# Kernel optimization log

Measured on AMD Instinct MI355X. Metric: run time of the kernel, lower is better.

Reference implementation:

```python
import jax, jax.numpy as jnp
import numpy as np

EMBED_DIM = 2048
NUM_HEADS = 16
HEAD_DIM = EMBED_DIM // NUM_HEADS
B, S = 1, 2048


def rotate_half(x):
    x1, x2 = jnp.split(x, 2, axis=-1)
    return jnp.concatenate((-x2, x1), axis=-1)


def setup_inputs() -> dict:
    key = jax.random.key(0)
    ks = jax.random.split(key, 8)
    scale = 1.0 / np.sqrt(EMBED_DIM)
    x = jax.random.normal(ks[0], (B, S, EMBED_DIM), dtype=jnp.float32)
    # realistic RoPE tables
    inv_freq = 1.0 / (10000.0 ** (jnp.arange(0, HEAD_DIM, 2, dtype=jnp.float32) / HEAD_DIM))
    t = jnp.arange(S, dtype=jnp.float32)
    freqs = jnp.outer(t, inv_freq)                      # [S, D/2]
    emb = jnp.concatenate((freqs, freqs), axis=-1)      # [S, D]
    rotary_cos = jnp.broadcast_to(jnp.cos(emb)[None], (B, S, HEAD_DIM))
    rotary_sin = jnp.broadcast_to(jnp.sin(emb)[None], (B, S, HEAD_DIM))
    Wq = jax.random.normal(ks[1], (EMBED_DIM, EMBED_DIM), dtype=jnp.float32) * scale
    Wk = jax.random.normal(ks[2], (EMBED_DIM, EMBED_DIM), dtype=jnp.float32) * scale
    Wv = jax.random.normal(ks[3], (EMBED_DIM, EMBED_DIM), dtype=jnp.float32) * scale
    Wo = jax.random.normal(ks[4], (EMBED_DIM, EMBED_DIM), dtype=jnp.float32) * scale
    return {"x": x, "rotary_cos": rotary_cos, "rotary_sin": rotary_sin,
            "Wq": Wq, "Wk": Wk, "Wv": Wv, "Wo": Wo}


def reference(x, rotary_cos, rotary_sin, Wq, Wk, Wv, Wo):
    b, s, e = x.shape
    h, d = NUM_HEADS, HEAD_DIM
    # QKV projections (nn.Linear: x @ W.T), reshape to [B, H, S, D]
    def proj(W):
        return jnp.einsum('bse,fe->bsf', x, W).reshape(b, s, h, d).transpose(0, 2, 1, 3)
    q, k, v = proj(Wq), proj(Wk), proj(Wv)
    # RoPE: cos/sin [B, S, D] -> [B, 1, S, D]
    cos = rotary_cos[:, None, :, :]
    sin = rotary_sin[:, None, :, :]
    q = q * cos + rotate_half(q) * sin
    k = k * cos + rotate_half(k) * sin
    # causal SDPA
    scores = jnp.einsum('bhqd,bhkd->bhqk', q, k) / jnp.sqrt(jnp.float32(d)).astype(x.dtype)
    causal = jnp.tril(jnp.ones((s, s), dtype=bool))
    scores = jnp.where(causal, scores, jnp.finfo(scores.dtype).min)
    attn = jax.nn.softmax(scores, axis=-1)
    out = jnp.einsum('bhqk,bhkd->bhqd', attn, v)
    out = out.transpose(0, 2, 1, 3).reshape(b, s, e)
    return jnp.einsum('bse,fe->bsf', out, Wo)
```

## Files before the change

### kernel.cpp

```cpp
#include <hip/hip_runtime.h>
#include <hip/hip_bf16.h>

#define S_LEN 2048
#define EMB   2048
#define NH    16
#define HD    128

typedef __attribute__((ext_vector_type(8))) __bf16 bf16x8;
typedef __attribute__((ext_vector_type(8))) unsigned short ushort8;
typedef __attribute__((ext_vector_type(4))) unsigned short ushort4v;
typedef __attribute__((ext_vector_type(4))) float  floatx4;

__device__ inline unsigned short f2b(float f) {
    __hip_bfloat16 h = __float2bfloat16(f);
    return *reinterpret_cast<unsigned short*>(&h);
}
__device__ inline float b2f(unsigned short u) {
    union { unsigned int i; float f; } c;
    c.i = ((unsigned int)u) << 16;
    return c.f;
}

__device__ inline ushort8 cvt16_lo(const float4& a, const float4& b) {
    ushort8 r;
    r[0] = f2b(a.x); r[1] = f2b(a.y); r[2] = f2b(a.z); r[3] = f2b(a.w);
    r[4] = f2b(b.x); r[5] = f2b(b.y); r[6] = f2b(b.z); r[7] = f2b(b.w);
    return r;
}

__global__ __launch_bounds__(256) void cvt_bf16x5(
    const float* __restrict__ s0, const float* __restrict__ s1,
    const float* __restrict__ s2, const float* __restrict__ s3,
    const float* __restrict__ s4,
    unsigned short* __restrict__ d0, unsigned short* __restrict__ d1,
    unsigned short* __restrict__ d2, unsigned short* __restrict__ d3,
    unsigned short* __restrict__ d4)
{
    const int i = blockIdx.x * 256 + threadIdx.x;
    const float* s; unsigned short* d;
    switch (blockIdx.y) {
        case 0: s = s0; d = d0; break;
        case 1: s = s1; d = d1; break;
        case 2: s = s2; d = d2; break;
        case 3: s = s3; d = d3; break;
        default: s = s4; d = d4; break;
    }
    float4 v = ((const float4*)s)[i];
    ushort4v r;
    r[0] = f2b(v.x); r[1] = f2b(v.y); r[2] = f2b(v.z); r[3] = f2b(v.w);
    ((ushort4v*)d)[i] = r;
}

template <int MODE, bool PRE>
__global__ __launch_bounds__(256) void gemm128(
    const void* __restrict__ Av,
    const void* __restrict__ B0v, const void* __restrict__ B1v,
    const void* __restrict__ B2v,
    float* __restrict__ outMN,
    __hip_bfloat16* __restrict__ qbuf, __hip_bfloat16* __restrict__ kbuf,
    __hip_bfloat16* __restrict__ vT,
    const float* __restrict__ rc, const float* __restrict__ rs)
{
    __shared__ union {
        struct { unsigned short A[128][40]; unsigned short B[128][40]; } s;
        unsigned short CtV[128][136];
        unsigned short CtR[128][137];
    } sm;

    const int m0 = blockIdx.x * 128;
    const int by = blockIdx.y;

    int widx = 0, hh = 0, n0 = 0;
    const void* Bv;
    if (MODE == 1) {
        widx = by >> 4;
        hh   = by & 15;
        n0   = hh * 128;
        Bv   = (widx == 0) ? B0v : (widx == 1) ? B1v : B2v;
    } else {
        n0 = by * 128;
        Bv = B0v;
    }

    const int t    = threadIdx.x;
    const int lane = t & 63;
    const int w    = t >> 6;
    const int l15  = lane & 15;
    const int g4   = lane >> 4;
    const int koff = g4 * 8;
    const int mw   = (w >> 1) * 64;
    const int nw   = (w & 1) * 64;

    const int srow = t >> 1;
    const int scol = (t & 1) * 16;

    const floatx4 z = {0.f, 0.f, 0.f, 0.f};
    floatx4 acc[4][4];
    #pragma unroll
    for (int i = 0; i < 4; i++)
        #pragma unroll
        for (int j = 0; j < 4; j++) acc[i][j] = z;

    const int K = EMB;
    for (int k0 = 0; k0 < K; k0 += 32) {
        ushort8 a0, a1, b0, b1;
        if (MODE == 0 || PRE) {
            const unsigned short* Ab = (const unsigned short*)Av;
            a0 = *(const ushort8*)(Ab + (size_t)(m0 + srow) * K + k0 + scol);
            a1 = *(const ushort8*)(Ab + (size_t)(m0 + srow) * K + k0 + scol + 8);
        } else {
            const float* Af = (const float*)Av;
            const float* ap = Af + (size_t)(m0 + srow) * K + k0 + scol;
            a0 = cvt16_lo(*(const float4*)(ap),     *(const float4*)(ap + 4));
            a1 = cvt16_lo(*(const float4*)(ap + 8), *(const float4*)(ap + 12));
        }
        if (PRE) {
            const unsigned short* Bb = (const unsigned short*)Bv;
            b0 = *(const ushort8*)(Bb + (size_t)(n0 + srow) * K + k0 + scol);
            b1 = *(const ushort8*)(Bb + (size_t)(n0 + srow) * K + k0 + scol + 8);
        } else {
            const float* Bf = (const float*)Bv;
            const float* bp = Bf + (size_t)(n0 + srow) * K + k0 + scol;
            b0 = cvt16_lo(*(const float4*)(bp),     *(const float4*)(bp + 4));
            b1 = cvt16_lo(*(const float4*)(bp + 8), *(const float4*)(bp + 12));
        }
        __syncthreads();
        *(ushort8*)&sm.s.A[srow][scol]     = a0;
        *(ushort8*)&sm.s.A[srow][scol + 8] = a1;
        *(ushort8*)&sm.s.B[srow][scol]     = b0;
        *(ushort8*)&sm.s.B[srow][scol + 8] = b1;
        __syncthreads();

        bf16x8 af[4], bg[4];
        #pragma unroll
        for (int i = 0; i < 4; i++)
            af[i] = *(const bf16x8*)&sm.s.A[mw + i * 16 + l15][koff];
        #pragma unroll
        for (int j = 0; j < 4; j++)
            bg[j] = *(const bf16x8*)&sm.s.B[nw + j * 16 + l15][koff];

        #pragma unroll
        for (int i = 0; i < 4; i++)
            #pragma unroll
            for (int j = 0; j < 4; j++)
                acc[i][j] = __builtin_amdgcn_mfma_f32_16x16x32_bf16(af[i], bg[j], acc[i][j], 0, 0, 0);
    }

    if (MODE == 0) {
        #pragma unroll
        for (int i = 0; i < 4; i++)
            #pragma unroll
            for (int j = 0; j < 4; j++)
                #pragma unroll
                for (int r = 0; r < 4; r++) {
                    int row = m0 + mw + i * 16 + g4 * 4 + r;
                    int col = n0 + nw + j * 16 + l15;
                    outMN[(size_t)row * EMB + col] = acc[i][j][r];
                }
    } else if (widx < 2) {
        __syncthreads();
        #pragma unroll
        for (int i = 0; i < 4; i++)
            #pragma unroll
            for (int j = 0; j < 4; j++)
                #pragma unroll
                for (int r = 0; r < 4; r++)
                    sm.CtR[nw + j * 16 + l15][mw + i * 16 + g4 * 4 + r] = f2b(acc[i][j][r]);
        __syncthreads();

        __hip_bfloat16* dst = (widx == 0) ? qbuf : kbuf;
        const int dd  = t & 127;
        const int sl0 = t >> 7;
        #pragma unroll 4
        for (int rep = 0; rep < 64; rep++) {
            const int sl = rep * 2 + sl0;
            const int s  = m0 + sl;
            const float c  = rc[(size_t)s * HD + dd];
            const float sn = rs[(size_t)s * HD + dd];
            const float x0 = b2f(sm.CtR[dd][sl]);
            const float xr = b2f(sm.CtR[dd ^ 64][sl]);
            const float rot = (dd < 64) ? -xr : xr;
            dst[((size_t)hh * S_LEN + s) * HD + dd] = __float2bfloat16(x0 * c + rot * sn);
        }
    } else {
        __syncthreads();
        #pragma unroll
        for (int i = 0; i < 4; i++)
            #pragma unroll
            for (int j = 0; j < 4; j++)
                #pragma unroll
                for (int r = 0; r < 4; r++)
                    sm.CtV[nw + j * 16 + l15][mw + i * 16 + g4 * 4 + r] = f2b(acc[i][j][r]);
        __syncthreads();
        const int dd = t >> 1;
        const int ms = (t & 1) * 64;
        __hip_bfloat16* dstv = vT + ((size_t)hh * HD + dd) * S_LEN + m0 + ms;
        #pragma unroll
        for (int c = 0; c < 8; c++)
            *(ushort8*)(dstv + c * 8) = *(const ushort8*)&sm.CtV[dd][ms + c * 8];
    }
}

__global__ __launch_bounds__(256) void flash_attn(
    const __hip_bfloat16* __restrict__ qb, const __hip_bfloat16* __restrict__ kb,
    const __hip_bfloat16* __restrict__ vT, __hip_bfloat16* __restrict__ attnb)
{
    __shared__ __align__(16) unsigned short Ks[64][136];
    __shared__ __align__(16) unsigned short Vs[128][72];
    __shared__ __align__(16) unsigned short Ps[4][16][72];

    const int bx = (gridDim.x - 1) - blockIdx.x;
    const int q0 = bx * 64;
    const int h  = blockIdx.y;
    const int t    = threadIdx.x;
    const int lane = t & 63;
    const int w    = t >> 6;
    const size_t hb  = (size_t)h * S_LEN;
    const size_t hbT = (size_t)h * HD;

    const int l15 = lane & 15;
    const int g4  = lane >> 4;
    const int koff = g4 * 8;

    const int kr = t >> 2;
    const int kc = (t & 3) * 32;
    const int vr = t >> 1;
    const int vc = (t & 1) * 32;

    bf16x8 qf[4];
    const __hip_bfloat16* qrow = qb + (hb + q0 + w * 16 + l15) * HD;
    #pragma unroll
    for (int kk = 0; kk < 4; kk++)
        qf[kk] = *(const bf16x8*)(qrow + kk * 32 + koff);

    const floatx4 z = {0.f, 0.f, 0.f, 0.f};
    floatx4 O[8] = {z, z, z, z, z, z, z, z};
    float lpart[4] = {0.f, 0.f, 0.f, 0.f};

    const float scale = 0.08838834764831845f;

    ushort8 krg[4], vrg[4];
    {
        const __hip_bfloat16* kg = kb + (hb + kr) * HD + kc;
        const __hip_bfloat16* vg = vT + (hbT + vr) * S_LEN + vc;
        #pragma unroll
        for (int c = 0; c < 4; c++) krg[c] = *(const ushort8*)(kg + c * 8);
        #pragma unroll
        for (int c = 0; c < 4; c++) vrg[c] = *(const ushort8*)(vg + c * 8);
    }

    for (int jb0 = 0; jb0 <= q0; jb0 += 64) {
        __syncthreads();
        #pragma unroll
        for (int c = 0; c < 4; c++) *(ushort8*)&Ks[kr][kc + c * 8] = krg[c];
        #pragma unroll
        for (int c = 0; c < 4; c++) *(ushort8*)&Vs[vr][vc + c * 8] = vrg[c];
        __syncthreads();

        if (jb0 + 64 <= q0) {
            const __hip_bfloat16* kg = kb + (hb + jb0 + 64 + kr) * HD + kc;
            const __hip_bfloat16* vg = vT + (hbT + vr) * S_LEN + jb0 + 64 + vc;
            #pragma unroll
            for (int c = 0; c < 4; c++) krg[c] = *(const ushort8*)(kg + c * 8);
            #pragma unroll
            for (int c = 0; c < 4; c++) vrg[c] = *(const ushort8*)(vg + c * 8);
        }

        floatx4 sc[4];
        #pragma unroll
        for (int jb = 0; jb < 4; jb++) {
            floatx4 acc = z;
            #pragma unroll
            for (int kk = 0; kk < 4; kk++) {
                bf16x8 kf = *(const bf16x8*)&Ks[jb * 16 + l15][kk * 32 + koff];
                acc = __builtin_amdgcn_mfma_f32_16x16x32_bf16(qf[kk], kf, acc, 0, 0, 0);
            }
            sc[jb] = acc;
        }

        const bool diag = (jb0 == q0);
        #pragma unroll
        for (int jb = 0; jb < 4; jb++)
            #pragma unroll
            for (int r = 0; r < 4; r++) {
                float s = sc[jb][r] * scale;
                if (diag && (jb * 16 + l15) > (w * 16 + g4 * 4 + r)) s = -1e30f;
                float p = __expf(s - 6.0f);
                sc[jb][r] = p;
                lpart[r] += p;
            }

        #pragma unroll
        for (int jb = 0; jb < 4; jb++)
            #pragma unroll
            for (int r = 0; r < 4; r++)
                Ps[w][g4 * 4 + r][jb * 16 + l15] = f2b(sc[jb][r]);

        #pragma unroll
        for (int half = 0; half < 2; half++) {
            bf16x8 af = *(const bf16x8*)&Ps[w][l15][half * 32 + koff];
            #pragma unroll
            for (int db = 0; db < 8; db++) {
                bf16x8 bf = *(const bf16x8*)&Vs[db * 16 + l15][half * 32 + koff];
                O[db] = __builtin_amdgcn_mfma_f32_16x16x32_bf16(af, bf, O[db], 0, 0, 0);
            }
        }
    }

    float inv[4];
    #pragma unroll
    for (int r = 0; r < 4; r++) {
        float s = lpart[r];
        #pragma unroll
        for (int o = 1; o < 16; o <<= 1) s += __shfl_xor(s, o, 64);
        inv[r] = 1.f / s;
    }

    #pragma unroll
    for (int db = 0; db < 8; db++)
        #pragma unroll
        for (int r = 0; r < 4; r++) {
            const int row = q0 + w * 16 + g4 * 4 + r;
            const int col = h * HD + db * 16 + l15;
            attnb[(size_t)row * EMB + col] = __float2bfloat16(O[db][r] * inv[r]);
        }
}

extern "C" void kernel_launch(void* const* d_in, const int* in_sizes, int n_in,
                              void* d_out, int out_size, void* d_ws, size_t ws_size,
                              hipStream_t stream) {
    const float* x  = (const float*)d_in[0];
    const float* rc = (const float*)d_in[1];
    const float* rs = (const float*)d_in[2];
    const float* Wq = (const float*)d_in[3];
    const float* Wk = (const float*)d_in[4];
    const float* Wv = (const float*)d_in[5];
    const float* Wo = (const float*)d_in[6];
    float* out = (float*)d_out;

    const size_t MB = 1u << 20;
    char* ws = (char*)d_ws;
    __hip_bfloat16* qbuf  = (__hip_bfloat16*)(ws);
    __hip_bfloat16* kbuf  = (__hip_bfloat16*)(ws +  8 * MB);
    __hip_bfloat16* vTbuf = (__hip_bfloat16*)(ws + 16 * MB);
    __hip_bfloat16* attnb = (__hip_bfloat16*)(ws + 24 * MB);

    const bool pre = (ws_size >= 72 * MB);

    if (pre) {
        unsigned short* xb  = (unsigned short*)(ws + 32 * MB);
        unsigned short* wqb = (unsigned short*)(ws + 40 * MB);
        unsigned short* wkb = (unsigned short*)(ws + 48 * MB);
        unsigned short* wvb = (unsigned short*)(ws + 56 * MB);
        unsigned short* wob = (unsigned short*)(ws + 64 * MB);

        hipLaunchKernelGGL(cvt_bf16x5, dim3(4096, 5), dim3(256), 0, stream,
                           x, Wq, Wk, Wv, Wo, xb, wqb, wkb, wvb, wob);

        hipLaunchKernelGGL((gemm128<1, true>), dim3(16, 48), dim3(256), 0, stream,
                           (const void*)xb, (const void*)wqb, (const void*)wkb,
                           (const void*)wvb, (float*)nullptr,
                           qbuf, kbuf, vTbuf, rc, rs);

        hipLaunchKernelGGL(flash_attn, dim3(S_LEN / 64, NH), dim3(256), 0, stream,
                           qbuf, kbuf, vTbuf, attnb);

        hipLaunchKernelGGL((gemm128<0, true>), dim3(16, 16), dim3(256), 0, stream,
                           (const void*)attnb, (const void*)wob, (const void*)nullptr,
                           (const void*)nullptr, out,
                           (__hip_bfloat16*)nullptr, (__hip_bfloat16*)nullptr,
                           (__hip_bfloat16*)nullptr, rc, rs);
    } else {
        hipLaunchKernelGGL((gemm128<1, false>), dim3(16, 48), dim3(256), 0, stream,
                           (const void*)x, (const void*)Wq, (const void*)Wk,
                           (const void*)Wv, (float*)nullptr,
                           qbuf, kbuf, vTbuf, rc, rs);

        hipLaunchKernelGGL(flash_attn, dim3(S_LEN / 64, NH), dim3(256), 0, stream,
                           qbuf, kbuf, vTbuf, attnb);

        hipLaunchKernelGGL((gemm128<0, false>), dim3(16, 16), dim3(256), 0, stream,
                           (const void*)attnb, (const void*)Wo, (const void*)nullptr,
                           (const void*)nullptr, out,
                           (__hip_bfloat16*)nullptr, (__hip_bfloat16*)nullptr,
                           (__hip_bfloat16*)nullptr, rc, rs);
    }
}
```

Before: 312.0 us.

## Use direct global-to-LDS loads with swizzle and split-K output projection

Replaces the register-staged tile loads in the pre-converted QKV and output GEMMs with global_load_lds direct-to-LDS transfers into an XOR-swizzled unpadded layout, cutting register traffic and LDS bank conflicts. The output projection is split along K into two halves that accumulate into a zeroed output with float atomics, doubling the block count to fill more CUs. This adds a memset and atomic-add traffic, makes the fp32 summation order nondeterministic, and still has no double buffering across the load/compute barrier.

```diff
diff --git a/kernel.cpp b/kernel.cpp
--- a/kernel.cpp
+++ b/kernel.cpp
@@ -26,6 +26,12 @@
     r[0] = f2b(a.x); r[1] = f2b(a.y); r[2] = f2b(a.z); r[3] = f2b(a.w);
     r[4] = f2b(b.x); r[5] = f2b(b.y); r[6] = f2b(b.z); r[7] = f2b(b.w);
     return r;
+}
+
+__device__ inline void gll16(const unsigned short* g, unsigned short* l) {
+    __builtin_amdgcn_global_load_lds(
+        (const __attribute__((address_space(1))) unsigned int*)g,
+        (__attribute__((address_space(3))) unsigned int*)l, 16, 0, 0);
 }
 
 __global__ __launch_bounds__(256) void cvt_bf16x5(
@@ -51,8 +57,190 @@
     ((ushort4v*)d)[i] = r;
 }
 
-template <int MODE, bool PRE>
-__global__ __launch_bounds__(256) void gemm128(
+
+__global__ __launch_bounds__(256) void gemm_qkv_async(
+    const unsigned short* __restrict__ Ab,
+    const unsigned short* __restrict__ Bq, const unsigned short* __restrict__ Bk,
+    const unsigned short* __restrict__ Bv,
+    __hip_bfloat16* __restrict__ qbuf, __hip_bfloat16* __restrict__ kbuf,
+    __hip_bfloat16* __restrict__ vT,
+    const float* __restrict__ rc, const float* __restrict__ rs)
+{
+    __shared__ __align__(16) union {
+        struct { unsigned short A[4096]; unsigned short B[4096]; } s;
+        unsigned short CtV[128][136];
+        unsigned short CtR[128][137];
+    } sm;
+
+    const int m0   = blockIdx.x * 128;
+    const int by   = blockIdx.y;
+    const int widx = by >> 4;
+    const int hh   = by & 15;
+    const int n0   = hh * 128;
+    const unsigned short* Bb = (widx == 0) ? Bq : (widx == 1) ? Bk : Bv;
+
+    const int t    = threadIdx.x;
+    const int lane = t & 63;
+    const int w    = t >> 6;
+    const int l15  = lane & 15;
+    const int g4   = lane >> 4;
+    const int mw   = (w >> 1) * 64;
+    const int nw   = (w & 1) * 64;
+
+    const int crow = lane >> 2;
+    const int clog = (lane & 3) ^ ((crow >> 1) & 3);
+    const int pc   = g4 ^ ((l15 >> 1) & 3);
+
+    const floatx4 z = {0.f, 0.f, 0.f, 0.f};
+    floatx4 acc[4][4];
+    #pragma unroll
+    for (int i = 0; i < 4; i++)
+        #pragma unroll
+        for (int j = 0; j < 4; j++) acc[i][j] = z;
+
+    const int K = EMB;
+    for (int k0 = 0; k0 < K; k0 += 32) {
+        __syncthreads();
+        #pragma unroll
+        for (int c = 0; c < 2; c++) {
+            const int ck  = w * 2 + c;
+            const int row = ck * 16 + crow;
+            gll16(Ab + (size_t)(m0 + row) * K + k0 + clog * 8, &sm.s.A[ck * 512]);
+            gll16(Bb + (size_t)(n0 + row) * K + k0 + clog * 8, &sm.s.B[ck * 512]);
+        }
+        __syncthreads();
+
+        bf16x8 af[4], bg[4];
+        #pragma unroll
+        for (int i = 0; i < 4; i++)
+            af[i] = *(const bf16x8*)&sm.s.A[(mw + i * 16 + l15) * 32 + pc * 8];
+        #pragma unroll
+        for (int j = 0; j < 4; j++)
+            bg[j] = *(const bf16x8*)&sm.s.B[(nw + j * 16 + l15) * 32 + pc * 8];
+
+        #pragma unroll
+        for (int i = 0; i < 4; i++)
+            #pragma unroll
+            for (int j = 0; j < 4; j++)
+                acc[i][j] = __builtin_amdgcn_mfma_f32_16x16x32_bf16(af[i], bg[j], acc[i][j], 0, 0, 0);
+    }
+
+    if (widx < 2) {
+        __syncthreads();
+        #pragma unroll
+        for (int i = 0; i < 4; i++)
+            #pragma unroll
+            for (int j = 0; j < 4; j++)
+                #pragma unroll
+                for (int r = 0; r < 4; r++)
+                    sm.CtR[nw + j * 16 + l15][mw + i * 16 + g4 * 4 + r] = f2b(acc[i][j][r]);
+        __syncthreads();
+
+        __hip_bfloat16* dst = (widx == 0) ? qbuf : kbuf;
+        const int dd  = t & 127;
+        const int sl0 = t >> 7;
+        #pragma unroll 4
+        for (int rep = 0; rep < 64; rep++) {
+            const int sl = rep * 2 + sl0;
+            const int s  = m0 + sl;
+            const float c  = rc[(size_t)s * HD + dd];
+            const float sn = rs[(size_t)s * HD + dd];
+            const float x0 = b2f(sm.CtR[dd][sl]);
+            const float xr = b2f(sm.CtR[dd ^ 64][sl]);
+            const float rot = (dd < 64) ? -xr : xr;
+            dst[((size_t)hh * S_LEN + s) * HD + dd] = __float2bfloat16(x0 * c + rot * sn);
+        }
+    } else {
+        __syncthreads();
+        #pragma unroll
+        for (int i = 0; i < 4; i++)
+            #pragma unroll
+            for (int j = 0; j < 4; j++)
+                #pragma unroll
+                for (int r = 0; r < 4; r++)
+                    sm.CtV[nw + j * 16 + l15][mw + i * 16 + g4 * 4 + r] = f2b(acc[i][j][r]);
+        __syncthreads();
+        const int dd = t >> 1;
+        const int ms = (t & 1) * 64;
+        __hip_bfloat16* dstv = vT + ((size_t)hh * HD + dd) * S_LEN + m0 + ms;
+        #pragma unroll
+        for (int c = 0; c < 8; c++)
+            *(ushort8*)(dstv + c * 8) = *(const ushort8*)&sm.CtV[dd][ms + c * 8];
+    }
+}
+
+__global__ __launch_bounds__(256) void gemm_wo_async(
+    const unsigned short* __restrict__ Ab,
+    const unsigned short* __restrict__ Bb,
+    float* __restrict__ outMN)
+{
+    __shared__ __align__(16) struct { unsigned short A[4096]; unsigned short B[4096]; } sm;
+
+    const int m0 = blockIdx.x * 128;
+    const int n0 = blockIdx.y * 128;
+    const int kz = blockIdx.z;
+
+    const int t    = threadIdx.x;
+    const int lane = t & 63;
+    const int w    = t >> 6;
+    const int l15  = lane & 15;
+    const int g4   = lane >> 4;
+    const int mw   = (w >> 1) * 64;
+    const int nw   = (w & 1) * 64;
+
+    const int crow = lane >> 2;
+    const int clog = (lane & 3) ^ ((crow >> 1) & 3);
+    const int pc   = g4 ^ ((l15 >> 1) & 3);
+
+    const floatx4 z = {0.f, 0.f, 0.f, 0.f};
+    floatx4 acc[4][4];
+    #pragma unroll
+    for (int i = 0; i < 4; i++)
+        #pragma unroll
+        for (int j = 0; j < 4; j++) acc[i][j] = z;
+
+    const int K = EMB;
+    const int kbeg = kz * (K / 2), kend = kbeg + K / 2;
+    for (int k0 = kbeg; k0 < kend; k0 += 32) {
+        __syncthreads();
+        #pragma unroll
+        for (int c = 0; c < 2; c++) {
+            const int ck  = w * 2 + c;
+            const int row = ck * 16 + crow;
+            gll16(Ab + (size_t)(m0 + row) * K + k0 + clog * 8, &sm.A[ck * 512]);
+            gll16(Bb + (size_t)(n0 + row) * K + k0 + clog * 8, &sm.B[ck * 512]);
+        }
+        __syncthreads();
+
+        bf16x8 af[4], bg[4];
+        #pragma unroll
+        for (int i = 0; i < 4; i++)
+            af[i] = *(const bf16x8*)&sm.A[(mw + i * 16 + l15) * 32 + pc * 8];
+        #pragma unroll
+        for (int j = 0; j < 4; j++)
+            bg[j] = *(const bf16x8*)&sm.B[(nw + j * 16 + l15) * 32 + pc * 8];
+
+        #pragma unroll
+        for (int i = 0; i < 4; i++)
+            #pragma unroll
+            for (int j = 0; j < 4; j++)
+                acc[i][j] = __builtin_amdgcn_mfma_f32_16x16x32_bf16(af[i], bg[j], acc[i][j], 0, 0, 0);
+    }
+
+    #pragma unroll
+    for (int i = 0; i < 4; i++)
+        #pragma unroll
+        for (int j = 0; j < 4; j++)
+            #pragma unroll
+            for (int r = 0; r < 4; r++) {
+                const int row = m0 + mw + i * 16 + g4 * 4 + r;
+                const int col = n0 + nw + j * 16 + l15;
+                atomicAdd(&outMN[(size_t)row * EMB + col], acc[i][j][r]);
+            }
+}
+
+template <int MODE>
+__global__ __launch_bounds__(256) void gemm128f(
     const void* __restrict__ Av,
     const void* __restrict__ B0v, const void* __restrict__ B1v,
     const void* __restrict__ B2v,
@@ -73,26 +261,14 @@
     int widx = 0, hh = 0, n0 = 0;
     const void* Bv;
     if (MODE == 1) {
-        widx = by >> 4;
-        hh   = by & 15;
-        n0   = hh * 128;
-        Bv   = (widx == 0) ? B0v : (widx == 1) ? B1v : B2v;
-    } else {
-        n0 = by * 128;
-        Bv = B0v;
-    }
-
-    const int t    = threadIdx.x;
-    const int lane = t & 63;
-    const int w    = t >> 6;
-    const int l15  = lane & 15;
-    const int g4   = lane >> 4;
-    const int koff = g4 * 8;
-    const int mw   = (w >> 1) * 64;
-    const int nw   = (w & 1) * 64;
-
-    const int srow = t >> 1;
-    const int scol = (t & 1) * 16;
+        widx = by >> 4; hh = by & 15; n0 = hh * 128;
+        Bv = (widx == 0) ? B0v : (widx == 1) ? B1v : B2v;
+    } else { n0 = by * 128; Bv = B0v; }
+
+    const int t = threadIdx.x, lane = t & 63, w = t >> 6;
+    const int l15 = lane & 15, g4 = lane >> 4, koff = g4 * 8;
+    const int mw = (w >> 1) * 64, nw = (w & 1) * 64;
+    const int srow = t >> 1, scol = (t & 1) * 16;
 
     const floatx4 z = {0.f, 0.f, 0.f, 0.f};
     floatx4 acc[4][4];
@@ -104,7 +280,7 @@
     const int K = EMB;
     for (int k0 = 0; k0 < K; k0 += 32) {
         ushort8 a0, a1, b0, b1;
-        if (MODE == 0 || PRE) {
+        if (MODE == 0) {
             const unsigned short* Ab = (const unsigned short*)Av;
             a0 = *(const ushort8*)(Ab + (size_t)(m0 + srow) * K + k0 + scol);
             a1 = *(const ushort8*)(Ab + (size_t)(m0 + srow) * K + k0 + scol + 8);
@@ -114,11 +290,7 @@
             a0 = cvt16_lo(*(const float4*)(ap),     *(const float4*)(ap + 4));
             a1 = cvt16_lo(*(const float4*)(ap + 8), *(const float4*)(ap + 12));
         }
-        if (PRE) {
-            const unsigned short* Bb = (const unsigned short*)Bv;
-            b0 = *(const ushort8*)(Bb + (size_t)(n0 + srow) * K + k0 + scol);
-            b1 = *(const ushort8*)(Bb + (size_t)(n0 + srow) * K + k0 + scol + 8);
-        } else {
+        {
             const float* Bf = (const float*)Bv;
             const float* bp = Bf + (size_t)(n0 + srow) * K + k0 + scol;
             b0 = cvt16_lo(*(const float4*)(bp),     *(const float4*)(bp + 4));
@@ -138,7 +310,6 @@
         #pragma unroll
         for (int j = 0; j < 4; j++)
             bg[j] = *(const bf16x8*)&sm.s.B[nw + j * 16 + l15][koff];
-
         #pragma unroll
         for (int i = 0; i < 4; i++)
             #pragma unroll
@@ -167,10 +338,8 @@
                 for (int r = 0; r < 4; r++)
                     sm.CtR[nw + j * 16 + l15][mw + i * 16 + g4 * 4 + r] = f2b(acc[i][j][r]);
         __syncthreads();
-
         __hip_bfloat16* dst = (widx == 0) ? qbuf : kbuf;
-        const int dd  = t & 127;
-        const int sl0 = t >> 7;
+        const int dd = t & 127, sl0 = t >> 7;
         #pragma unroll 4
         for (int rep = 0; rep < 64; rep++) {
             const int sl = rep * 2 + sl0;
@@ -192,8 +361,7 @@
                 for (int r = 0; r < 4; r++)
                     sm.CtV[nw + j * 16 + l15][mw + i * 16 + g4 * 4 + r] = f2b(acc[i][j][r]);
         __syncthreads();
-        const int dd = t >> 1;
-        const int ms = (t & 1) * 64;
+        const int dd = t >> 1, ms = (t & 1) * 64;
         __hip_bfloat16* dstv = vT + ((size_t)hh * HD + dd) * S_LEN + m0 + ms;
         #pragma unroll
         for (int c = 0; c < 8; c++)
@@ -354,24 +522,21 @@
         unsigned short* wvb = (unsigned short*)(ws + 56 * MB);
         unsigned short* wob = (unsigned short*)(ws + 64 * MB);
 
+        hipMemsetAsync(out, 0, (size_t)S_LEN * EMB * sizeof(float), stream);
+
         hipLaunchKernelGGL(cvt_bf16x5, dim3(4096, 5), dim3(256), 0, stream,
                            x, Wq, Wk, Wv, Wo, xb, wqb, wkb, wvb, wob);
 
-        hipLaunchKernelGGL((gemm128<1, true>), dim3(16, 48), dim3(256), 0, stream,
-                           (const void*)xb, (const void*)wqb, (const void*)wkb,
-                           (const void*)wvb, (float*)nullptr,
-                           qbuf, kbuf, vTbuf, rc, rs);
+        hipLaunchKernelGGL(gemm_qkv_async, dim3(16, 48), dim3(256), 0, stream,
+                           xb, wqb, wkb, wvb, qbuf, kbuf, vTbuf, rc, rs);
 
         hipLaunchKernelGGL(flash_attn, dim3(S_LEN / 64, NH), dim3(256), 0, stream,
                            qbuf, kbuf, vTbuf, attnb);
 
-        hipLaunchKernelGGL((gemm128<0, true>), dim3(16, 16), dim3(256), 0, stream,
-                           (const void*)attnb, (const void*)wob, (const void*)nullptr,
-                           (const void*)nullptr, out,
-                           (__hip_bfloat16*)nullptr, (__hip_bfloat16*)nullptr,
-                           (__hip_bfloat16*)nullptr, rc, rs);
+        hipLaunchKernelGGL(gemm_wo_async, dim3(16, 16, 2), dim3(256), 0, stream,
+                           (const unsigned short*)attnb, wob, out);
     } else {
-        hipLaunchKernelGGL((gemm128<1, false>), dim3(16, 48), dim3(256), 0, stream,
+        hipLaunchKernelGGL((gemm128f<1>), dim3(16, 48), dim3(256), 0, stream,
                            (const void*)x, (const void*)Wq, (const void*)Wk,
                            (const void*)Wv, (float*)nullptr,
                            qbuf, kbuf, vTbuf, rc, rs);
@@ -379,7 +544,7 @@
         hipLaunchKernelGGL(flash_attn, dim3(S_LEN / 64, NH), dim3(256), 0, stream,
                            qbuf, kbuf, vTbuf, attnb);
 
-        hipLaunchKernelGGL((gemm128<0, false>), dim3(16, 16), dim3(256), 0, stream,
+        hipLaunchKernelGGL((gemm128f<0>), dim3(16, 16), dim3(256), 0, stream,
                            (const void*)attnb, (const void*)Wo, (const void*)nullptr,
                            (const void*)nullptr, out,
                            (__hip_bfloat16*)nullptr, (__hip_bfloat16*)nullptr,
```

Result: no change. 313.1 us (+0.4%).
